# Kernel optimization log

Measured on AMD Instinct MI355X. Metric: run time of the kernel, lower is better.

Reference implementation:

```python
import jax, jax.numpy as jnp
import numpy as np

EPS = 1e-12  # matches torch F.normalize eps


def setup_inputs() -> dict:
    key = jax.random.key(0)
    k1, k2, k3 = jax.random.split(key, 3)
    N, C, H, W, K = 16, 1024, 32, 32, 32
    x = jax.random.normal(k1, (N, C, H, W), dtype=jnp.float32)
    # 1x1 conv weight (K, C, 1, 1) stored as (K, C)
    conv_w = jax.random.normal(k2, (K, C), dtype=jnp.float32) * 0.02
    centroids = jax.random.uniform(k3, (K, C), dtype=jnp.float32)
    return {"x": x, "conv_w": conv_w, "centroids": centroids}


def _l2norm(v, axis):
    return v / jnp.maximum(jnp.linalg.norm(v, axis=axis, keepdims=True), EPS)


def reference(x, conv_w, centroids):
    N, C, H, W = x.shape
    K = centroids.shape[0]
    # normalize_input: L2 over channel dim
    x = _l2norm(x, axis=1)
    xf = x.reshape(N, C, H * W)                      # (N, C, P)
    # 1x1 conv == per-pixel matmul -> (N, K, P)
    logits = jnp.einsum('kc,ncp->nkp', conv_w, xf)
    a = jax.nn.softmax(logits, axis=1)               # softmax over clusters
    # sum_p a[n,k,p] * (x[n,:,p] - centroids[k,:])
    # == (a @ x^T) - (sum_p a) * centroids  (two GEMMs, no (N,K,C,P) blowup)
    vlad = jnp.einsum('nkp,ncp->nkc', a, xf) - a.sum(-1)[:, :, None] * centroids[None]
    vlad = _l2norm(vlad, axis=2)                     # intra-cluster L2 norm
    vlad = vlad.reshape(N, K * C)
    vlad = _l2norm(vlad, axis=1)                     # global L2 norm
    return vlad
```

## Files before the change

### kernel.cpp

```cpp
#include <hip/hip_runtime.h>

#define NB   16
#define CC   1024
#define PP   1024
#define KK   32
#define EPSF 1e-12f

typedef __attribute__((ext_vector_type(8))) short  bf16x8;
typedef __attribute__((ext_vector_type(4))) float  f32x4;

__device__ __forceinline__ float bf2f(unsigned short u) {
    union { unsigned int i; float f; } v; v.i = ((unsigned int)u) << 16; return v.f;
}
__device__ __forceinline__ unsigned short f2bf(float f) {
    union { float f; unsigned int i; } v; v.f = f;
    return (unsigned short)((v.i + 0x7fffu + ((v.i >> 16) & 1u)) >> 16);
}

template <typename T> struct IO;
template <> struct IO<float> {
    static __device__ __forceinline__ float  ld (const float* p) { return *p; }
    static __device__ __forceinline__ float4 ld4(const float* p) { return *(const float4*)p; }
};
template <> struct IO<unsigned short> {
    static __device__ __forceinline__ float  ld (const unsigned short* p) { return bf2f(*p); }
    static __device__ __forceinline__ float4 ld4(const unsigned short* p) {
        const ushort4 u = *(const ushort4*)p;
        return make_float4(bf2f(u.x), bf2f(u.y), bf2f(u.z), bf2f(u.w));
    }
};

__global__ __launch_bounds__(256) void k_detect(const unsigned short* __restrict__ xu,
                                                int* __restrict__ flag) {
    __shared__ int s;
    const int t = threadIdx.x;
    if (t == 0) s = 0;
    __syncthreads();
    int bad = 0;
    for (int i = t; i < 4096; i += 256)
        if (((xu[i] >> 7) & 0xFFu) > 0x9Fu) bad = 1;
    if (bad) atomicOr(&s, 1);
    __syncthreads();
    if (t == 0) flag[0] = s;
}

template <typename T>
__device__ __forceinline__ void attn_body(const T* __restrict__ x,
                                          const T* __restrict__ w,
                                          float* __restrict__ rnorm_ws,
                                          unsigned short* __restrict__ attn_g,
                                          float* __restrict__ asum) {
    __shared__ __align__(16) unsigned short xt[32 * 136];
    __shared__ __align__(16) unsigned short w_lds[32 * 136];
    __shared__ float red[32 * 32];
    __shared__ float lg[32 * 33];
    __shared__ float inv_lds[32];
    __shared__ float rnorm_lds[32];
    const int b = blockIdx.x, t = threadIdx.x;
    const int n = b >> 5, pbase = (b & 31) * 32;
    const int lane = t & 63, wv = t >> 6;
    const int quad = lane >> 4, l15 = lane & 15;
    const int mt = wv & 1, nt = wv >> 1;

    const size_t xb = (size_t)n * CC * PP + pbase;
    float ss0 = 0.f, ss1 = 0.f, ss2 = 0.f, ss3 = 0.f;
    f32x4 acc = {0.f, 0.f, 0.f, 0.f};

    const int pxg = 4 * (t & 7);
    const int crow = t >> 3;

    for (int ch = 0; ch < 8; ++ch) {
        const int c0 = ch * 128;
        __syncthreads();
        #pragma unroll
        for (int pass = 0; pass < 4; ++pass) {
            const int cl = crow + 32 * pass;
            const float4 v = IO<T>::ld4(&x[xb + (size_t)(c0 + cl) * PP + pxg]);
            ss0 += v.x * v.x; ss1 += v.y * v.y; ss2 += v.z * v.z; ss3 += v.w * v.w;
            xt[(pxg + 0) * 136 + cl] = f2bf(v.x);
            xt[(pxg + 1) * 136 + cl] = f2bf(v.y);
            xt[(pxg + 2) * 136 + cl] = f2bf(v.z);
            xt[(pxg + 3) * 136 + cl] = f2bf(v.w);
        }
        {
            const int k = t >> 3, cg = (t & 7) * 16;
            #pragma unroll
            for (int j = 0; j < 4; ++j) {
                const float4 v = IO<T>::ld4(&w[k * CC + c0 + cg + 4 * j]);
                ushort4 u;
                u.x = f2bf(v.x); u.y = f2bf(v.y); u.z = f2bf(v.z); u.w = f2bf(v.w);
                *(ushort4*)&w_lds[k * 136 + cg + 4 * j] = u;
            }
        }
        __syncthreads();
        #pragma unroll
        for (int ks = 0; ks < 4; ++ks) {
            const bf16x8 av = *(const bf16x8*)&xt[(mt * 16 + l15) * 136 + ks * 32 + quad * 8];
            const bf16x8 bv = *(const bf16x8*)&w_lds[(nt * 16 + l15) * 136 + ks * 32 + quad * 8];
            acc = __builtin_amdgcn_mfma_f32_16x16x32_bf16(av, bv, acc, 0, 0, 0);
        }
    }
    red[crow * 32 + pxg + 0] = ss0;
    red[crow * 32 + pxg + 1] = ss1;
    red[crow * 32 + pxg + 2] = ss2;
    red[crow * 32 + pxg + 3] = ss3;
    __syncthreads();
    if (t < 32) {
        float s = 0.f;
        #pragma unroll
        for (int g = 0; g < 32; ++g) s += red[g * 32 + t];
        const float r = 1.0f / fmaxf(sqrtf(s), EPSF);
        rnorm_lds[t] = r;
        rnorm_ws[n * PP + pbase + t] = r;
    }
    __syncthreads();
    #pragma unroll
    for (int reg = 0; reg < 4; ++reg) {
        const int px = mt * 16 + quad * 4 + reg;
        lg[px * 33 + nt * 16 + l15] = acc[reg] * rnorm_lds[px];
    }
    __syncthreads();
    if (t < 32) {
        float m = -1e30f;
        #pragma unroll
        for (int k = 0; k < KK; ++k) m = fmaxf(m, lg[t * 33 + k]);
        float s = 0.f;
        #pragma unroll
        for (int k = 0; k < KK; ++k) {
            const float e = expf(lg[t * 33 + k] - m);
            lg[t * 33 + k] = e;
            s += e;
        }
        inv_lds[t] = 1.0f / s;
    }
    __syncthreads();
    {
        const int k = t >> 3;
        float s = 0.f;
        ushort4 u;
        float vv[4];
        #pragma unroll
        for (int j = 0; j < 4; ++j) {
            const int px = pxg + j;
            vv[j] = lg[px * 33 + k] * inv_lds[px];
        }
        u.x = f2bf(vv[0]); u.y = f2bf(vv[1]); u.z = f2bf(vv[2]); u.w = f2bf(vv[3]);
        s = bf2f(u.x) + bf2f(u.y) + bf2f(u.z) + bf2f(u.w);
        *(ushort4*)&attn_g[((size_t)n * KK + k) * PP + pbase + pxg] = u;
        s += __shfl_xor(s, 1, 64);
        s += __shfl_xor(s, 2, 64);
        s += __shfl_xor(s, 4, 64);
        if ((t & 7) == 0) atomicAdd(&asum[n * KK + k], s);
    }
}
__global__ __launch_bounds__(256) void k_attn(const void* __restrict__ x,
                                              const void* __restrict__ w,
                                              const int* __restrict__ flag,
                                              float* __restrict__ rnorm_ws,
                                              unsigned short* __restrict__ attn_g,
                                              float* __restrict__ asum) {
    if (*flag) attn_body<float>((const float*)x, (const float*)w, rnorm_ws, attn_g, asum);
    else       attn_body<unsigned short>((const unsigned short*)x, (const unsigned short*)w,
                                         rnorm_ws, attn_g, asum);
}

template <typename T>
__device__ __forceinline__ void vlad_body(const T* __restrict__ x,
                                          const T* __restrict__ cent,
                                          const float* __restrict__ rnorm_ws,
                                          const unsigned short* __restrict__ attn_g,
                                          const float* __restrict__ asum,
                                          float* __restrict__ vlad,
                                          float* __restrict__ ssqnk) {
    __shared__ __align__(16) unsigned short xt[64 * 136];
    __shared__ __align__(16) unsigned short at_lds[32 * 136];
    __shared__ float asum_lds[32];
    __shared__ float ssq_lds[32];
    const int b = blockIdx.x, t = threadIdx.x;
    const int n = b >> 4, cbase = (b & 15) * 64;
    const int lane = t & 63, wv = t >> 6;
    const int quad = lane >> 4, l15 = lane & 15;
    const int mt = wv & 1, nt0 = (wv >> 1) * 2, nt1 = nt0 + 1;

    if (t < 32) { asum_lds[t] = asum[n * KK + t]; ssq_lds[t] = 0.f; }

    f32x4 acc0 = {0.f, 0.f, 0.f, 0.f}, acc1 = {0.f, 0.f, 0.f, 0.f};
    const size_t xb = (size_t)n * CC * PP + (size_t)cbase * PP;

    for (int pc = 0; pc < 8; ++pc) {
        const int p0 = pc * 128;
        __syncthreads();
        {
            const int k = t >> 3, pg = (t & 7) * 16;
            const size_t base = ((size_t)n * KK + k) * PP + p0 + pg;
            const uint4 u0 = *(const uint4*)&attn_g[base];
            const uint4 u1 = *(const uint4*)&attn_g[base + 8];
            *(uint4*)&at_lds[k * 136 + pg]     = u0;
            *(uint4*)&at_lds[k * 136 + pg + 8] = u1;
        }
        {
            const int pg = 4 * (t & 31);
            const float4 rn = *(const float4*)&rnorm_ws[n * PP + p0 + pg];
            #pragma unroll
            for (int pass = 0; pass < 8; ++pass) {
                const int ci = (t >> 5) + 8 * pass;
                const float4 v = IO<T>::ld4(&x[xb + (size_t)ci * PP + p0 + pg]);
                ushort4 u;
                u.x = f2bf(v.x * rn.x); u.y = f2bf(v.y * rn.y);
                u.z = f2bf(v.z * rn.z); u.w = f2bf(v.w * rn.w);
                *(ushort4*)&xt[ci * 136 + pg] = u;
            }
        }
        __syncthreads();
        #pragma unroll
        for (int ks = 0; ks < 4; ++ks) {
            const bf16x8 av  = *(const bf16x8*)&at_lds[(mt * 16 + l15) * 136 + ks * 32 + quad * 8];
            const bf16x8 bv0 = *(const bf16x8*)&xt[(nt0 * 16 + l15) * 136 + ks * 32 + quad * 8];
            const bf16x8 bv1 = *(const bf16x8*)&xt[(nt1 * 16 + l15) * 136 + ks * 32 + quad * 8];
            acc0 = __builtin_amdgcn_mfma_f32_16x16x32_bf16(av, bv0, acc0, 0, 0, 0);
            acc1 = __builtin_amdgcn_mfma_f32_16x16x32_bf16(av, bv1, acc1, 0, 0, 0);
        }
    }
    __syncthreads();
    const int c0g = cbase + nt0 * 16 + l15, c1g = cbase + nt1 * 16 + l15;
    #pragma unroll
    for (int reg = 0; reg < 4; ++reg) {
        const int k = mt * 16 + quad * 4 + reg;
        const float A = asum_lds[k];
        const float v0 = acc0[reg] - A * IO<T>::ld(&cent[k * CC + c0g]);
        const float v1 = acc1[reg] - A * IO<T>::ld(&cent[k * CC + c1g]);
        vlad[((size_t)n * KK + k) * CC + c0g] = v0;
        vlad[((size_t)n * KK + k) * CC + c1g] = v1;
        float s = v0 * v0 + v1 * v1;
        s += __shfl_xor(s, 1, 64);
        s += __shfl_xor(s, 2, 64);
        s += __shfl_xor(s, 4, 64);
        s += __shfl_xor(s, 8, 64);
        if (l15 == 0) atomicAdd(&ssq_lds[k], s);
    }
    __syncthreads();
    if (t < 32) atomicAdd(&ssqnk[n * KK + t], ssq_lds[t]);
}
__global__ __launch_bounds__(256) void k_vlad(const void* __restrict__ x,
                                              const void* __restrict__ cent,
                                              const int* __restrict__ flag,
                                              const float* __restrict__ rnorm_ws,
                                              const unsigned short* __restrict__ attn_g,
                                              const float* __restrict__ asum,
                                              float* __restrict__ vlad,
                                              float* __restrict__ ssqnk) {
    if (*flag) vlad_body<float>((const float*)x, (const float*)cent, rnorm_ws, attn_g,
                                asum, vlad, ssqnk);
    else       vlad_body<unsigned short>((const unsigned short*)x, (const unsigned short*)cent,
                                         rnorm_ws, attn_g, asum, vlad, ssqnk);
}

__global__ __launch_bounds__(64) void k_factors(const float* __restrict__ ssqnk,
                                                float* __restrict__ rintra,
                                                float* __restrict__ rglob) {
    const int n = blockIdx.x, t = threadIdx.x;
    const float s = (t < KK) ? ssqnk[n * KK + t] : 0.f;
    const float r = 1.0f / fmaxf(sqrtf(s), EPSF);
    if (t < KK) rintra[n * KK + t] = r;
    float g = s * r * r;
    for (int off = 32; off > 0; off >>= 1) g += __shfl_down(g, off, 64);
    if (t == 0) rglob[n] = 1.0f / fmaxf(sqrtf(g), EPSF);
}

__global__ __launch_bounds__(256) void k_out(const float* __restrict__ vlad,
                                             const float* __restrict__ rintra,
                                             const float* __restrict__ rglob,
                                             const int* __restrict__ flag,
                                             void* __restrict__ out) {
    const int b = blockIdx.x, t = threadIdx.x;
    const float f = rintra[b] * rglob[b >> 5];
    const float4 v = ((const float4*)(vlad + (size_t)b * CC))[t];
    if (*flag) {
        float4 o; o.x = v.x * f; o.y = v.y * f; o.z = v.z * f; o.w = v.w * f;
        ((float4*)((float*)out + (size_t)b * CC))[t] = o;
    } else {
        ushort4 u;
        u.x = f2bf(v.x * f); u.y = f2bf(v.y * f);
        u.z = f2bf(v.z * f); u.w = f2bf(v.w * f);
        ((ushort4*)((unsigned short*)out + (size_t)b * CC))[t] = u;
    }
}

extern "C" void kernel_launch(void* const* d_in, const int* in_sizes, int n_in,
                              void* d_out, int out_size, void* d_ws, size_t ws_size,
                              hipStream_t stream) {
    const void* x    = d_in[0];
    const void* w    = d_in[1];
    const void* cent = d_in[2];

    float* ws       = (float*)d_ws;
    float* rnorm_ws = ws;
    float* vlad     = rnorm_ws + NB * PP;
    float* asum     = vlad + NB * KK * CC;
    float* ssqnk    = asum + NB * KK;
    float* rintra   = ssqnk + NB * KK;
    float* rglob    = rintra + NB * KK;
    int*   flag     = (int*)(rglob + NB);
    unsigned short* attn_g = (unsigned short*)(flag + 4);

    hipMemsetAsync(asum, 0, 2 * NB * KK * sizeof(float), stream);

    k_detect<<<1, 256, 0, stream>>>((const unsigned short*)x, flag);
    k_attn<<<NB * 32, 256, 0, stream>>>(x, w, flag, rnorm_ws, attn_g, asum);
    k_vlad<<<NB * 16, 256, 0, stream>>>(x, cent, flag, rnorm_ws, attn_g, asum, vlad, ssqnk);
    k_factors<<<NB, 64, 0, stream>>>(ssqnk, rintra, rglob);
    k_out<<<NB * KK, 256, 0, stream>>>(vlad, rintra, rglob, flag, d_out);
}
```

Baseline: 125.5 us.

## Precompute normalized bf16 x, its transpose and weights in a separate pass

Adds a k_norm pass that computes per-pixel L2 norms and writes normalized bf16 copies of x in both channel-major and pixel-major layouts, plus a bf16 copy of the conv weight. The attention and VLAD GEMM kernels then stage plain bf16 tiles with 16-byte loads instead of converting and transposing fp32 data on the fly. The VLAD kernel is retiled to 32-channel blocks with one accumulator per wave, which doubles the grid. In exchange, x is read three times in the new pass and two large bf16 intermediates are written and read back, so total memory traffic grows substantially.

```diff
diff --git a/kernel.cpp b/kernel.cpp
--- a/kernel.cpp
+++ b/kernel.cpp
@@ -8,13 +8,14 @@
 
 typedef __attribute__((ext_vector_type(8))) short  bf16x8;
 typedef __attribute__((ext_vector_type(4))) float  f32x4;
-
-__device__ __forceinline__ float bf2f(unsigned short u) {
+typedef unsigned short us;
+
+__device__ __forceinline__ float bf2f(us u) {
     union { unsigned int i; float f; } v; v.i = ((unsigned int)u) << 16; return v.f;
 }
-__device__ __forceinline__ unsigned short f2bf(float f) {
+__device__ __forceinline__ us f2bf(float f) {
     union { float f; unsigned int i; } v; v.f = f;
-    return (unsigned short)((v.i + 0x7fffu + ((v.i >> 16) & 1u)) >> 16);
+    return (us)((v.i + 0x7fffu + ((v.i >> 16) & 1u)) >> 16);
 }
 
 template <typename T> struct IO;
@@ -22,15 +23,15 @@
     static __device__ __forceinline__ float  ld (const float* p) { return *p; }
     static __device__ __forceinline__ float4 ld4(const float* p) { return *(const float4*)p; }
 };
-template <> struct IO<unsigned short> {
-    static __device__ __forceinline__ float  ld (const unsigned short* p) { return bf2f(*p); }
-    static __device__ __forceinline__ float4 ld4(const unsigned short* p) {
+template <> struct IO<us> {
+    static __device__ __forceinline__ float  ld (const us* p) { return bf2f(*p); }
+    static __device__ __forceinline__ float4 ld4(const us* p) {
         const ushort4 u = *(const ushort4*)p;
         return make_float4(bf2f(u.x), bf2f(u.y), bf2f(u.z), bf2f(u.w));
     }
 };
 
-__global__ __launch_bounds__(256) void k_detect(const unsigned short* __restrict__ xu,
+__global__ __launch_bounds__(256) void k_detect(const us* __restrict__ xu,
                                                 int* __restrict__ flag) {
     __shared__ int s;
     const int t = threadIdx.x;
@@ -45,79 +46,120 @@
 }
 
 template <typename T>
-__device__ __forceinline__ void attn_body(const T* __restrict__ x,
+__device__ __forceinline__ void norm_body(const T* __restrict__ x,
                                           const T* __restrict__ w,
-                                          float* __restrict__ rnorm_ws,
-                                          unsigned short* __restrict__ attn_g,
-                                          float* __restrict__ asum) {
-    __shared__ __align__(16) unsigned short xt[32 * 136];
-    __shared__ __align__(16) unsigned short w_lds[32 * 136];
-    __shared__ float red[32 * 32];
+                                          us* __restrict__ xhat,
+                                          us* __restrict__ xhatT,
+                                          us* __restrict__ what) {
+    const int b = blockIdx.x, t = threadIdx.x;
+    if (b >= NB * 32) {
+        const int base = (b - NB * 32) * 2048 + t * 8;
+        const float4 v0 = IO<T>::ld4(w + base);
+        const float4 v1 = IO<T>::ld4(w + base + 4);
+        ushort4 u0, u1;
+        u0.x = f2bf(v0.x); u0.y = f2bf(v0.y); u0.z = f2bf(v0.z); u0.w = f2bf(v0.w);
+        u1.x = f2bf(v1.x); u1.y = f2bf(v1.y); u1.z = f2bf(v1.z); u1.w = f2bf(v1.w);
+        *(ushort4*)&what[base]     = u0;
+        *(ushort4*)&what[base + 4] = u1;
+        return;
+    }
+    __shared__ float red[32 * 33];
+    __shared__ float rn[32];
+    const int n = b >> 5, pbase = (b & 31) * 32;
+    const int a = t & 7, crow = t >> 3;
+    const int pxg = 4 * a;
+    const size_t xb = (size_t)n * CC * PP + pbase;
+    float s0 = 0.f, s1 = 0.f, s2 = 0.f, s3 = 0.f;
+    for (int i = 0; i < 32; ++i) {
+        const int c = crow + 32 * i;
+        const float4 v = IO<T>::ld4(x + xb + (size_t)c * PP + pxg);
+        s0 += v.x * v.x; s1 += v.y * v.y; s2 += v.z * v.z; s3 += v.w * v.w;
+    }
+    red[crow * 33 + pxg + 0] = s0;
+    red[crow * 33 + pxg + 1] = s1;
+    red[crow * 33 + pxg + 2] = s2;
+    red[crow * 33 + pxg + 3] = s3;
+    __syncthreads();
+    if (t < 32) {
+        float s = 0.f;
+        #pragma unroll
+        for (int g = 0; g < 32; ++g) s += red[g * 33 + t];
+        rn[t] = 1.0f / fmaxf(sqrtf(s), EPSF);
+    }
+    __syncthreads();
+    const float r0 = rn[pxg], r1 = rn[pxg + 1], r2 = rn[pxg + 2], r3 = rn[pxg + 3];
+    for (int i = 0; i < 32; ++i) {
+        const int c = crow + 32 * i;
+        const float4 v = IO<T>::ld4(x + xb + (size_t)c * PP + pxg);
+        ushort4 u;
+        u.x = f2bf(v.x * r0); u.y = f2bf(v.y * r1);
+        u.z = f2bf(v.z * r2); u.w = f2bf(v.w * r3);
+        *(ushort4*)&xhat[((size_t)n * CC + c) * PP + pbase + pxg] = u;
+    }
+    const int px = t & 31, cq = t >> 5;
+    const float rpx = rn[px];
+    const size_t tb = ((size_t)n * PP + pbase + px) * CC;
+    for (int i = 0; i < 32; ++i) {
+        const int c4 = 4 * (cq + 8 * i);
+        const float v0 = IO<T>::ld(x + xb + (size_t)(c4 + 0) * PP + px);
+        const float v1 = IO<T>::ld(x + xb + (size_t)(c4 + 1) * PP + px);
+        const float v2 = IO<T>::ld(x + xb + (size_t)(c4 + 2) * PP + px);
+        const float v3 = IO<T>::ld(x + xb + (size_t)(c4 + 3) * PP + px);
+        ushort4 u;
+        u.x = f2bf(v0 * rpx); u.y = f2bf(v1 * rpx);
+        u.z = f2bf(v2 * rpx); u.w = f2bf(v3 * rpx);
+        *(ushort4*)&xhatT[tb + c4] = u;
+    }
+}
+__global__ __launch_bounds__(256) void k_norm(const void* __restrict__ x,
+                                              const void* __restrict__ w,
+                                              const int* __restrict__ flag,
+                                              us* __restrict__ xhat,
+                                              us* __restrict__ xhatT,
+                                              us* __restrict__ what) {
+    if (*flag) norm_body<float>((const float*)x, (const float*)w, xhat, xhatT, what);
+    else       norm_body<us>((const us*)x, (const us*)w, xhat, xhatT, what);
+}
+
+__global__ __launch_bounds__(256) void k_attn(const us* __restrict__ xhatT,
+                                              const us* __restrict__ what,
+                                              us* __restrict__ attn_g,
+                                              float* __restrict__ asum) {
+    __shared__ __align__(16) us xt[32 * 136];
     __shared__ float lg[32 * 33];
     __shared__ float inv_lds[32];
-    __shared__ float rnorm_lds[32];
     const int b = blockIdx.x, t = threadIdx.x;
     const int n = b >> 5, pbase = (b & 31) * 32;
     const int lane = t & 63, wv = t >> 6;
     const int quad = lane >> 4, l15 = lane & 15;
-    const int mt = wv & 1, nt = wv >> 1;
-
-    const size_t xb = (size_t)n * CC * PP + pbase;
-    float ss0 = 0.f, ss1 = 0.f, ss2 = 0.f, ss3 = 0.f;
+    const int mt = wv >> 1, ntk = wv & 1;
+
     f32x4 acc = {0.f, 0.f, 0.f, 0.f};
-
-    const int pxg = 4 * (t & 7);
-    const int crow = t >> 3;
+    const size_t xtb = ((size_t)n * PP + pbase) * CC;
 
     for (int ch = 0; ch < 8; ++ch) {
         const int c0 = ch * 128;
         __syncthreads();
         #pragma unroll
-        for (int pass = 0; pass < 4; ++pass) {
-            const int cl = crow + 32 * pass;
-            const float4 v = IO<T>::ld4(&x[xb + (size_t)(c0 + cl) * PP + pxg]);
-            ss0 += v.x * v.x; ss1 += v.y * v.y; ss2 += v.z * v.z; ss3 += v.w * v.w;
-            xt[(pxg + 0) * 136 + cl] = f2bf(v.x);
-            xt[(pxg + 1) * 136 + cl] = f2bf(v.y);
-            xt[(pxg + 2) * 136 + cl] = f2bf(v.z);
-            xt[(pxg + 3) * 136 + cl] = f2bf(v.w);
-        }
-        {
-            const int k = t >> 3, cg = (t & 7) * 16;
-            #pragma unroll
-            for (int j = 0; j < 4; ++j) {
-                const float4 v = IO<T>::ld4(&w[k * CC + c0 + cg + 4 * j]);
-                ushort4 u;
-                u.x = f2bf(v.x); u.y = f2bf(v.y); u.z = f2bf(v.z); u.w = f2bf(v.w);
-                *(ushort4*)&w_lds[k * 136 + cg + 4 * j] = u;
-            }
+        for (int s = 0; s < 2; ++s) {
+            const int idx = t + 256 * s;
+            const int px = idx >> 4, unit = idx & 15;
+            const uint4 u = *(const uint4*)&xhatT[xtb + (size_t)px * CC + c0 + unit * 8];
+            *(uint4*)&xt[px * 136 + unit * 8] = u;
         }
         __syncthreads();
         #pragma unroll
         for (int ks = 0; ks < 4; ++ks) {
             const bf16x8 av = *(const bf16x8*)&xt[(mt * 16 + l15) * 136 + ks * 32 + quad * 8];
-            const bf16x8 bv = *(const bf16x8*)&w_lds[(nt * 16 + l15) * 136 + ks * 32 + quad * 8];
+            const bf16x8 bv = *(const bf16x8*)&what[(ntk * 16 + l15) * CC + c0 + ks * 32 + quad * 8];
             acc = __builtin_amdgcn_mfma_f32_16x16x32_bf16(av, bv, acc, 0, 0, 0);
         }
-    }
-    red[crow * 32 + pxg + 0] = ss0;
-    red[crow * 32 + pxg + 1] = ss1;
-    red[crow * 32 + pxg + 2] = ss2;
-    red[crow * 32 + pxg + 3] = ss3;
-    __syncthreads();
-    if (t < 32) {
-        float s = 0.f;
-        #pragma unroll
-        for (int g = 0; g < 32; ++g) s += red[g * 32 + t];
-        const float r = 1.0f / fmaxf(sqrtf(s), EPSF);
-        rnorm_lds[t] = r;
-        rnorm_ws[n * PP + pbase + t] = r;
     }
     __syncthreads();
     #pragma unroll
     for (int reg = 0; reg < 4; ++reg) {
         const int px = mt * 16 + quad * 4 + reg;
-        lg[px * 33 + nt * 16 + l15] = acc[reg] * rnorm_lds[px];
+        lg[px * 33 + ntk * 16 + l15] = acc[reg];
     }
     __syncthreads();
     if (t < 32) {
@@ -135,124 +177,87 @@
     }
     __syncthreads();
     {
-        const int k = t >> 3;
-        float s = 0.f;
+        const int k = t >> 3, ps = (t & 7) * 4;
         ushort4 u;
-        float vv[4];
+        float sum = 0.f;
         #pragma unroll
         for (int j = 0; j < 4; ++j) {
-            const int px = pxg + j;
-            vv[j] = lg[px * 33 + k] * inv_lds[px];
-        }
-        u.x = f2bf(vv[0]); u.y = f2bf(vv[1]); u.z = f2bf(vv[2]); u.w = f2bf(vv[3]);
-        s = bf2f(u.x) + bf2f(u.y) + bf2f(u.z) + bf2f(u.w);
-        *(ushort4*)&attn_g[((size_t)n * KK + k) * PP + pbase + pxg] = u;
-        s += __shfl_xor(s, 1, 64);
-        s += __shfl_xor(s, 2, 64);
-        s += __shfl_xor(s, 4, 64);
-        if ((t & 7) == 0) atomicAdd(&asum[n * KK + k], s);
-    }
-}
-__global__ __launch_bounds__(256) void k_attn(const void* __restrict__ x,
-                                              const void* __restrict__ w,
-                                              const int* __restrict__ flag,
-                                              float* __restrict__ rnorm_ws,
-                                              unsigned short* __restrict__ attn_g,
-                                              float* __restrict__ asum) {
-    if (*flag) attn_body<float>((const float*)x, (const float*)w, rnorm_ws, attn_g, asum);
-    else       attn_body<unsigned short>((const unsigned short*)x, (const unsigned short*)w,
-                                         rnorm_ws, attn_g, asum);
+            const int px = ps + j;
+            const us e = f2bf(lg[px * 33 + k] * inv_lds[px]);
+            ((us*)&u)[j] = e;
+            sum += bf2f(e);
+        }
+        *(ushort4*)&attn_g[((size_t)n * KK + k) * PP + pbase + ps] = u;
+        sum += __shfl_down(sum, 1, 64);
+        sum += __shfl_down(sum, 2, 64);
+        sum += __shfl_down(sum, 4, 64);
+        if ((t & 7) == 0) atomicAdd(&asum[n * KK + k], sum);
+    }
 }
 
 template <typename T>
-__device__ __forceinline__ void vlad_body(const T* __restrict__ x,
+__device__ __forceinline__ void vlad_body(const us* __restrict__ xhat,
+                                          const us* __restrict__ attn_g,
                                           const T* __restrict__ cent,
-                                          const float* __restrict__ rnorm_ws,
-                                          const unsigned short* __restrict__ attn_g,
                                           const float* __restrict__ asum,
                                           float* __restrict__ vlad,
                                           float* __restrict__ ssqnk) {
-    __shared__ __align__(16) unsigned short xt[64 * 136];
-    __shared__ __align__(16) unsigned short at_lds[32 * 136];
+    __shared__ __align__(16) us xc[32 * 136];
     __shared__ float asum_lds[32];
-    __shared__ float ssq_lds[32];
     const int b = blockIdx.x, t = threadIdx.x;
-    const int n = b >> 4, cbase = (b & 15) * 64;
+    const int n = b >> 5, cb = (b & 31) * 32;
     const int lane = t & 63, wv = t >> 6;
     const int quad = lane >> 4, l15 = lane & 15;
-    const int mt = wv & 1, nt0 = (wv >> 1) * 2, nt1 = nt0 + 1;
-
-    if (t < 32) { asum_lds[t] = asum[n * KK + t]; ssq_lds[t] = 0.f; }
-
-    f32x4 acc0 = {0.f, 0.f, 0.f, 0.f}, acc1 = {0.f, 0.f, 0.f, 0.f};
-    const size_t xb = (size_t)n * CC * PP + (size_t)cbase * PP;
-
-    for (int pc = 0; pc < 8; ++pc) {
-        const int p0 = pc * 128;
+    const int mtk = wv >> 1, ntc = wv & 1;
+
+    if (t < 32) asum_lds[t] = asum[n * KK + t];
+
+    f32x4 acc = {0.f, 0.f, 0.f, 0.f};
+    const size_t xb = ((size_t)n * CC + cb) * PP;
+    const size_t ab = ((size_t)n * KK + mtk * 16 + l15) * PP;
+
+    for (int ch = 0; ch < 8; ++ch) {
+        const int p0 = ch * 128;
         __syncthreads();
-        {
-            const int k = t >> 3, pg = (t & 7) * 16;
-            const size_t base = ((size_t)n * KK + k) * PP + p0 + pg;
-            const uint4 u0 = *(const uint4*)&attn_g[base];
-            const uint4 u1 = *(const uint4*)&attn_g[base + 8];
-            *(uint4*)&at_lds[k * 136 + pg]     = u0;
-            *(uint4*)&at_lds[k * 136 + pg + 8] = u1;
-        }
-        {
-            const int pg = 4 * (t & 31);
-            const float4 rn = *(const float4*)&rnorm_ws[n * PP + p0 + pg];
-            #pragma unroll
-            for (int pass = 0; pass < 8; ++pass) {
-                const int ci = (t >> 5) + 8 * pass;
-                const float4 v = IO<T>::ld4(&x[xb + (size_t)ci * PP + p0 + pg]);
-                ushort4 u;
-                u.x = f2bf(v.x * rn.x); u.y = f2bf(v.y * rn.y);
-                u.z = f2bf(v.z * rn.z); u.w = f2bf(v.w * rn.w);
-                *(ushort4*)&xt[ci * 136 + pg] = u;
-            }
+        #pragma unroll
+        for (int s = 0; s < 2; ++s) {
+            const int idx = t + 256 * s;
+            const int ci = idx >> 4, unit = idx & 15;
+            const uint4 u = *(const uint4*)&xhat[xb + (size_t)ci * PP + p0 + unit * 8];
+            *(uint4*)&xc[ci * 136 + unit * 8] = u;
         }
         __syncthreads();
         #pragma unroll
         for (int ks = 0; ks < 4; ++ks) {
-            const bf16x8 av  = *(const bf16x8*)&at_lds[(mt * 16 + l15) * 136 + ks * 32 + quad * 8];
-            const bf16x8 bv0 = *(const bf16x8*)&xt[(nt0 * 16 + l15) * 136 + ks * 32 + quad * 8];
-            const bf16x8 bv1 = *(const bf16x8*)&xt[(nt1 * 16 + l15) * 136 + ks * 32 + quad * 8];
-            acc0 = __builtin_amdgcn_mfma_f32_16x16x32_bf16(av, bv0, acc0, 0, 0, 0);
-            acc1 = __builtin_amdgcn_mfma_f32_16x16x32_bf16(av, bv1, acc1, 0, 0, 0);
-        }
-    }
-    __syncthreads();
-    const int c0g = cbase + nt0 * 16 + l15, c1g = cbase + nt1 * 16 + l15;
+            const bf16x8 av = *(const bf16x8*)&attn_g[ab + p0 + ks * 32 + quad * 8];
+            const bf16x8 bv = *(const bf16x8*)&xc[(ntc * 16 + l15) * 136 + ks * 32 + quad * 8];
+            acc = __builtin_amdgcn_mfma_f32_16x16x32_bf16(av, bv, acc, 0, 0, 0);
+        }
+    }
+    const int cg = cb + ntc * 16 + l15;
     #pragma unroll
     for (int reg = 0; reg < 4; ++reg) {
-        const int k = mt * 16 + quad * 4 + reg;
+        const int k = mtk * 16 + quad * 4 + reg;
         const float A = asum_lds[k];
-        const float v0 = acc0[reg] - A * IO<T>::ld(&cent[k * CC + c0g]);
-        const float v1 = acc1[reg] - A * IO<T>::ld(&cent[k * CC + c1g]);
-        vlad[((size_t)n * KK + k) * CC + c0g] = v0;
-        vlad[((size_t)n * KK + k) * CC + c1g] = v1;
-        float s = v0 * v0 + v1 * v1;
+        const float v = acc[reg] - A * IO<T>::ld(&cent[k * CC + cg]);
+        vlad[((size_t)n * KK + k) * CC + cg] = v;
+        float s = v * v;
         s += __shfl_xor(s, 1, 64);
         s += __shfl_xor(s, 2, 64);
         s += __shfl_xor(s, 4, 64);
         s += __shfl_xor(s, 8, 64);
-        if (l15 == 0) atomicAdd(&ssq_lds[k], s);
-    }
-    __syncthreads();
-    if (t < 32) atomicAdd(&ssqnk[n * KK + t], ssq_lds[t]);
-}
-__global__ __launch_bounds__(256) void k_vlad(const void* __restrict__ x,
+        if (l15 == 0) atomicAdd(&ssqnk[n * KK + k], s);
+    }
+}
+__global__ __launch_bounds__(256) void k_vlad(const us* __restrict__ xhat,
+                                              const us* __restrict__ attn_g,
                                               const void* __restrict__ cent,
                                               const int* __restrict__ flag,
-                                              const float* __restrict__ rnorm_ws,
-                                              const unsigned short* __restrict__ attn_g,
                                               const float* __restrict__ asum,
                                               float* __restrict__ vlad,
                                               float* __restrict__ ssqnk) {
-    if (*flag) vlad_body<float>((const float*)x, (const float*)cent, rnorm_ws, attn_g,
-                                asum, vlad, ssqnk);
-    else       vlad_body<unsigned short>((const unsigned short*)x, (const unsigned short*)cent,
-                                         rnorm_ws, attn_g, asum, vlad, ssqnk);
+    if (*flag) vlad_body<float>(xhat, attn_g, (const float*)cent, asum, vlad, ssqnk);
+    else       vlad_body<us>(xhat, attn_g, (const us*)cent, asum, vlad, ssqnk);
 }
 
 __global__ __launch_bounds__(64) void k_factors(const float* __restrict__ ssqnk,
@@ -282,7 +287,7 @@
         ushort4 u;
         u.x = f2bf(v.x * f); u.y = f2bf(v.y * f);
         u.z = f2bf(v.z * f); u.w = f2bf(v.w * f);
-        ((ushort4*)((unsigned short*)out + (size_t)b * CC))[t] = u;
+        ((ushort4*)((us*)out + (size_t)b * CC))[t] = u;
     }
 }
 
@@ -293,21 +298,24 @@
     const void* w    = d_in[1];
     const void* cent = d_in[2];
 
-    float* ws       = (float*)d_ws;
-    float* rnorm_ws = ws;
-    float* vlad     = rnorm_ws + NB * PP;
-    float* asum     = vlad + NB * KK * CC;
-    float* ssqnk    = asum + NB * KK;
-    float* rintra   = ssqnk + NB * KK;
-    float* rglob    = rintra + NB * KK;
-    int*   flag     = (int*)(rglob + NB);
-    unsigned short* attn_g = (unsigned short*)(flag + 4);
+    float* ws     = (float*)d_ws;
+    float* vlad   = ws;
+    float* asum   = vlad + 524288;
+    float* ssqnk  = asum + 512;
+    float* rintra = ssqnk + 512;
+    float* rglob  = rintra + 512;
+    int*   flag   = (int*)(rglob + 16);
+    us* attn_g = (us*)(flag + 4);
+    us* xhat   = attn_g + 524288;
+    us* xhatT  = xhat + 16777216;
+    us* what   = xhatT + 16777216;
 
     hipMemsetAsync(asum, 0, 2 * NB * KK * sizeof(float), stream);
 
-    k_detect<<<1, 256, 0, stream>>>((const unsigned short*)x, flag);
-    k_attn<<<NB * 32, 256, 0, stream>>>(x, w, flag, rnorm_ws, attn_g, asum);
-    k_vlad<<<NB * 16, 256, 0, stream>>>(x, cent, flag, rnorm_ws, attn_g, asum, vlad, ssqnk);
+    k_detect<<<1, 256, 0, stream>>>((const us*)x, flag);
+    k_norm<<<NB * 32 + 16, 256, 0, stream>>>(x, w, flag, xhat, xhatT, what);
+    k_attn<<<NB * 32, 256, 0, stream>>>(xhatT, what, attn_g, asum);
+    k_vlad<<<NB * 32, 256, 0, stream>>>(xhat, attn_g, cent, flag, asum, vlad, ssqnk);
     k_factors<<<NB, 64, 0, stream>>>(ssqnk, rintra, rglob);
     k_out<<<NB * KK, 256, 0, stream>>>(vlad, rintra, rglob, flag, d_out);
 }
```

Result: slower. 201.9 us (+60.9%).
